# Performance work log

Hardware: AMD Instinct MI355X
Metric: run time of the kernel (lower is better)

## Reference

```python
import jax, jax.numpy as jnp
import numpy as np

NCHW = ('NCHW', 'OIHW', 'NCHW')


def _conv3x3_same(x, w, b):
    # ZeroPad2d(1) + 3x3 valid conv == 3x3 conv with padding 1
    y = jax.lax.conv_general_dilated(x, w, window_strides=(1, 1),
                                     padding=((1, 1), (1, 1)),
                                     dimension_numbers=NCHW)
    return y + b[None, :, None, None]


def _maxpool2(x):
    return jax.lax.reduce_window(x, -jnp.inf, jax.lax.max,
                                 (1, 1, 2, 2), (1, 1, 2, 2), 'VALID')


def setup_inputs() -> dict:
    key = jax.random.key(0)
    ks = jax.random.split(key, 12)
    B, T1, T2, R, D = 1, 512, 512, 9, 3840
    q = jax.random.normal(ks[0], (B, T1, R, D), jnp.float32)
    t = jax.random.normal(ks[1], (B, T2, R, D), jnp.float32)
    # ViSiL features are L2-normalized region descriptors -> sims in [-1,1]
    q = q / jnp.linalg.norm(q, axis=-1, keepdims=True)
    t = t / jnp.linalg.norm(t, axis=-1, keepdims=True)
    s = 0.05
    return {
        'query': q, 'target': t,
        'w1': jax.random.normal(ks[2], (32, 1, 3, 3), jnp.float32) * s,
        'b1': jax.random.normal(ks[3], (32,), jnp.float32) * s,
        'w2': jax.random.normal(ks[4], (64, 32, 3, 3), jnp.float32) * s,
        'b2': jax.random.normal(ks[5], (64,), jnp.float32) * s,
        'w3': jax.random.normal(ks[6], (128, 64, 3, 3), jnp.float32) * s,
        'b3': jax.random.normal(ks[7], (128,), jnp.float32) * s,
        'wf': jax.random.normal(ks[8], (1, 128, 1, 1), jnp.float32) * s,
        'bf': jax.random.normal(ks[9], (1,), jnp.float32) * s,
    }


def reference(query, target, w1, b1, w2, b2, w3, b3, wf, bf):
    # frame-to-frame: region-pair similarity [B,T1,O,P,T2]
    sim5 = jnp.einsum('biok,bjpk->biopj', query, target)
    # Chamfer (axes=[3,2]): max over target regions P, mean over query regions O
    f2f = jnp.mean(jnp.max(sim5, axis=3), axis=2)  # [B,T1,T2]
    # video comperator CNN
    x = f2f[:, None]                                 # [B,1,T1,T2]
    x = _maxpool2(jax.nn.relu(_conv3x3_same(x, w1, b1)))
    x = _maxpool2(jax.nn.relu(_conv3x3_same(x, w2, b2)))
    x = jax.nn.relu(_conv3x3_same(x, w3, b3))
    x = jax.lax.conv_general_dilated(x, wf, (1, 1), ((0, 0), (0, 0)),
                                     dimension_numbers=NCHW)
    x = x + bf[None, :, None, None]
    s = jnp.clip(x[:, 0], -1.0, 1.0)                 # Hardtanh, [B,H,W]
    # video-to-video Chamfer (axes=[2,1]): max over axis 2, mean over axis 1
    return jnp.mean(jnp.max(s, axis=2), axis=1)      # [B]
```

## Files before the change

### kernel.cpp

```cpp
#include <hip/hip_runtime.h>
#include <hip/hip_bf16.h>

typedef float f32x4 __attribute__((ext_vector_type(4)));
typedef int v8i __attribute__((ext_vector_type(8)));

#define AS3 __attribute__((address_space(3)))
#define AS1 __attribute__((address_space(1)))

__global__ __launch_bounds__(256) void cvt_fp8_kernel(const float* __restrict__ src,
                                                      unsigned int* __restrict__ dst,
                                                      int n16) {
  int idx = blockIdx.x * 256 + threadIdx.x;
  if (idx >= n16) return;
  const float4* s4 = (const float4*)src;
  uint4 o;
  unsigned int* op = (unsigned int*)&o;
#pragma unroll
  for (int i = 0; i < 4; ++i) {
    float4 v = s4[idx * 4 + i];
    int w = 0;
    w = __builtin_amdgcn_cvt_pk_fp8_f32(v.x * 16.f, v.y * 16.f, w, false);
    w = __builtin_amdgcn_cvt_pk_fp8_f32(v.z * 16.f, v.w * 16.f, w, true);
    op[i] = w;
  }
  ((uint4*)dst)[idx] = o;
}

__global__ __launch_bounds__(768) void gemm_cmax_kernel(const unsigned char* __restrict__ qf8,
                                                        const unsigned char* __restrict__ tf8,
                                                        float* __restrict__ cmax) {
  __shared__ __align__(16) char smem[147456];
  const int tid  = threadIdx.x;
  const int wv   = tid >> 6;
  const int lane = tid & 63;
  const int quad = lane >> 4;
  const int l16  = lane & 15;
  const int wrow = wv >> 1, wcol = wv & 1;
  const int bi = blockIdx.y, bj = blockIdx.x;

  f32x4 acc[3][9];
#pragma unroll
  for (int a = 0; a < 3; ++a)
#pragma unroll
    for (int b = 0; b < 9; ++b) acc[a][b] = (f32x4){0.f, 0.f, 0.f, 0.f};

  const unsigned char* gptr[6];
#pragma unroll
  for (int r = 0; r < 6; ++r) {
    int s   = r * 768 + wv * 64 + lane;
    int mat = (s >= 2304);
    int sm  = s - mat * 2304;
    int row = sm >> 3, pc = sm & 7;
    int gc  = pc ^ (row & 7);
    const unsigned char* base = mat ? (tf8 + (size_t)(bj * 288 + row) * 3840)
                                    : (qf8 + (size_t)(bi * 288 + row) * 3840);
    gptr[r] = base + gc * 16;
  }

  int buf = 0;
#pragma unroll
  for (int r = 0; r < 6; ++r)
    __builtin_amdgcn_global_load_lds((const AS1 void*)(gptr[r]),
                                     (AS3 void*)(smem + (r * 768 + wv * 64) * 16), 16, 0, 0);

  const int arow0 = wrow * 48 + l16;
  const int bcol0 = wcol * 144 + l16;

  for (int kt = 0; kt < 30; ++kt) {
    __syncthreads();
    if (kt < 29) {
      int nb = buf ^ 1;
#pragma unroll
      for (int r = 0; r < 6; ++r)
        __builtin_amdgcn_global_load_lds((const AS1 void*)(gptr[r] + (kt + 1) * 128),
                                         (AS3 void*)(smem + nb * 73728 + (r * 768 + wv * 64) * 16),
                                         16, 0, 0);
    }
    const char* A = smem + buf * 73728;
    const char* B = A + 36864;

    v8i av[3];
#pragma unroll
    for (int sr = 0; sr < 3; ++sr) {
      int row = arow0 + sr * 16;
      int sw  = row & 7;
      int p0  = (quad * 2) ^ sw, p1 = (quad * 2 + 1) ^ sw;
      int4 lo = *(const int4*)(A + row * 128 + p0 * 16);
      int4 hi = *(const int4*)(A + row * 128 + p1 * 16);
      v8i v;
      v[0] = lo.x; v[1] = lo.y; v[2] = lo.z; v[3] = lo.w;
      v[4] = hi.x; v[5] = hi.y; v[6] = hi.z; v[7] = hi.w;
      av[sr] = v;
    }
#pragma unroll
    for (int c = 0; c < 9; ++c) {
      int col = bcol0 + c * 16;
      int sw  = col & 7;
      int p0  = (quad * 2) ^ sw, p1 = (quad * 2 + 1) ^ sw;
      int4 lo = *(const int4*)(B + col * 128 + p0 * 16);
      int4 hi = *(const int4*)(B + col * 128 + p1 * 16);
      v8i bv;
      bv[0] = lo.x; bv[1] = lo.y; bv[2] = lo.z; bv[3] = lo.w;
      bv[4] = hi.x; bv[5] = hi.y; bv[6] = hi.z; bv[7] = hi.w;
      acc[0][c] = __builtin_amdgcn_mfma_scale_f32_16x16x128_f8f6f4(
          av[0], bv, acc[0][c], 0, 0, 0, 0x7f7f7f7f, 0, 0x7f7f7f7f);
      acc[1][c] = __builtin_amdgcn_mfma_scale_f32_16x16x128_f8f6f4(
          av[1], bv, acc[1][c], 0, 0, 0, 0x7f7f7f7f, 0, 0x7f7f7f7f);
      acc[2][c] = __builtin_amdgcn_mfma_scale_f32_16x16x128_f8f6f4(
          av[2], bv, acc[2][c], 0, 0, 0, 0x7f7f7f7f, 0, 0x7f7f7f7f);
    }
    buf ^= 1;
  }

  __syncthreads();
  float* scr = (float*)smem;
#pragma unroll
  for (int b = 0; b < 18; ++b) {
    const int bw = b / 3, bs = b - bw * 3;
    if (wrow == bw) {
#pragma unroll
      for (int c = 0; c < 9; ++c)
#pragma unroll
        for (int r = 0; r < 4; ++r)
          scr[(quad * 4 + r) * 288 + wcol * 144 + c * 16 + l16] = acc[bs][c][r] * (1.f / 256.f);
    }
    __syncthreads();
    if (tid < 512) {
      int row = tid >> 5, jg = tid & 31;
      const float* p = scr + row * 288 + jg * 9;
      float m = p[0];
#pragma unroll
      for (int k = 1; k < 9; ++k) m = fmaxf(m, p[k]);
      cmax[(size_t)(bi * 288 + b * 16 + row) * 512 + bj * 32 + jg] = m;
    }
    __syncthreads();
  }
}

__global__ __launch_bounds__(512) void mean9_kernel(const float* __restrict__ cmax,
                                                    float* __restrict__ f2f) {
  int i = blockIdx.x, j = threadIdx.x;
  float s = 0.f;
#pragma unroll
  for (int o = 0; o < 9; ++o) s += cmax[(size_t)(i * 9 + o) * 512 + j];
  f2f[i * 512 + j] = s * (1.f / 9.f);
}

__global__ __launch_bounds__(256) void conv1_kernel(const float* __restrict__ in,
                                                    const float* __restrict__ w1,
                                                    const float* __restrict__ b1,
                                                    float* __restrict__ out) {
  __shared__ float tile[34 * 36];
  __shared__ float wl[320];
  int t = blockIdx.x;
  int ty0 = (t >> 4) * 32, tx0 = (t & 15) * 32;
  int py = threadIdx.x >> 4, px = threadIdx.x & 15;

  for (int idx = threadIdx.x; idx < 320; idx += 256)
    wl[idx] = (idx < 288) ? w1[idx] : b1[idx - 288];
  for (int idx = threadIdx.x; idx < 34 * 34; idx += 256) {
    int r = idx / 34, c = idx % 34;
    int gy = ty0 + r - 1, gx = tx0 + c - 1;
    tile[r * 36 + c] = ((unsigned)gy < 512u && (unsigned)gx < 512u) ? in[gy * 512 + gx] : 0.f;
  }
  __syncthreads();

  float win[4][4];
#pragma unroll
  for (int r = 0; r < 4; ++r)
#pragma unroll
    for (int c = 0; c < 4; ++c)
      win[r][c] = tile[(2 * py + r) * 36 + 2 * px + c];

  int gy2 = (t >> 4) * 16 + py, gx2 = (t & 15) * 16 + px;
#pragma unroll 1
  for (int ch = 0; ch < 32; ++ch) {
    float w[9];
#pragma unroll
    for (int k = 0; k < 9; ++k) w[k] = wl[ch * 9 + k];
    float m = -INFINITY;
#pragma unroll
    for (int a = 0; a < 2; ++a)
#pragma unroll
      for (int b = 0; b < 2; ++b) {
        float s = 0.f;
#pragma unroll
        for (int ky = 0; ky < 3; ++ky)
#pragma unroll
          for (int kx = 0; kx < 3; ++kx) s += win[a + ky][b + kx] * w[ky * 3 + kx];
        m = fmaxf(m, s);
      }
    out[ch * 65536 + gy2 * 256 + gx2] = fmaxf(m + wl[288 + ch], 0.f);
  }
}

__global__ __launch_bounds__(256) void conv2_kernel(const float* __restrict__ in,
                                                    const float* __restrict__ w2,
                                                    const float* __restrict__ b2,
                                                    float* __restrict__ out) {
  __shared__ __align__(16) float wlds[32 * 4 * 12];
  __shared__ float tile[2][2][34 * 36];
  const int tid = threadIdx.x;
  int cog = blockIdx.x >> 6;
  int t   = blockIdx.x & 63;
  int ty0 = (t >> 3) * 32, tx0 = (t & 7) * 32;
  int py = tid >> 4, px = tid & 15;

  for (int idx = tid; idx < 1152; idx += 256) {
    int co = idx / 288, rem = idx % 288, ci = rem / 9, k = rem % 9;
    wlds[(ci * 4 + co) * 12 + k] = w2[((cog * 4 + co) * 32 + ci) * 9 + k];
  }
  for (int idx = tid; idx < 2312; idx += 256) {
    int pl = idx / 1156, rc = idx % 1156, r = rc / 34, c = rc % 34;
    int gy = ty0 + r - 1, gx = tx0 + c - 1;
    tile[0][pl][r * 36 + c] = ((unsigned)gy < 256u && (unsigned)gx < 256u)
                                  ? in[pl * 65536 + gy * 256 + gx] : 0.f;
  }
  __syncthreads();

  float acc[4][4];
#pragma unroll
  for (int p = 0; p < 4; ++p)
#pragma unroll
    for (int co = 0; co < 4; ++co) acc[p][co] = 0.f;

#pragma unroll 1
  for (int cb = 0; cb < 16; ++cb) {
    int buf = cb & 1;
    float pf[10];
    if (cb < 15) {
#pragma unroll
      for (int i = 0; i < 10; ++i) {
        int idx = tid + i * 256;
        float v = 0.f;
        if (idx < 2312) {
          int pl = idx / 1156, rc = idx % 1156, r = rc / 34, c = rc % 34;
          int gy = ty0 + r - 1, gx = tx0 + c - 1;
          if ((unsigned)gy < 256u && (unsigned)gx < 256u)
            v = in[((cb + 1) * 2 + pl) * 65536 + gy * 256 + gx];
        }
        pf[i] = v;
      }
    }
#pragma unroll
    for (int pl = 0; pl < 2; ++pl) {
      float win[4][4];
#pragma unroll
      for (int r = 0; r < 4; ++r) {
        float2 lo = *(const float2*)&tile[buf][pl][(2 * py + r) * 36 + 2 * px];
        float2 hi = *(const float2*)&tile[buf][pl][(2 * py + r) * 36 + 2 * px + 2];
        win[r][0] = lo.x; win[r][1] = lo.y; win[r][2] = hi.x; win[r][3] = hi.y;
      }
      int ci = cb * 2 + pl;
#pragma unroll
      for (int co = 0; co < 4; ++co) {
        const float* wp = &wlds[(ci * 4 + co) * 12];
        float4 w0 = *(const float4*)wp;
        float4 w1v = *(const float4*)(wp + 4);
        float w8 = wp[8];
        float w[9] = {w0.x, w0.y, w0.z, w0.w, w1v.x, w1v.y, w1v.z, w1v.w, w8};
#pragma unroll
        for (int a = 0; a < 2; ++a)
#pragma unroll
          for (int b = 0; b < 2; ++b) {
            float s = acc[a * 2 + b][co];
#pragma unroll
            for (int ky = 0; ky < 3; ++ky)
#pragma unroll
              for (int kx = 0; kx < 3; ++kx) s += win[a + ky][b + kx] * w[ky * 3 + kx];
            acc[a * 2 + b][co] = s;
          }
      }
    }
    if (cb < 15) {
#pragma unroll
      for (int i = 0; i < 10; ++i) {
        int idx = tid + i * 256;
        if (idx < 2312) {
          int pl = idx / 1156, rc = idx % 1156, r = rc / 34, c = rc % 34;
          tile[buf ^ 1][pl][r * 36 + c] = pf[i];
        }
      }
    }
    __syncthreads();
  }

  int gy2 = (t >> 3) * 16 + py, gx2 = (t & 7) * 16 + px;
#pragma unroll
  for (int co = 0; co < 4; ++co) {
    float m = fmaxf(fmaxf(acc[0][co], acc[1][co]), fmaxf(acc[2][co], acc[3][co]));
    out[(cog * 4 + co) * 16384 + gy2 * 128 + gx2] = fmaxf(m + b2[cog * 4 + co], 0.f);
  }
}

__global__ __launch_bounds__(256) void conv3_kernel(const float* __restrict__ in,
                                                    const float* __restrict__ w3,
                                                    const float* __restrict__ b3,
                                                    float* __restrict__ out) {
  __shared__ __align__(16) float wlds[64 * 4 * 12];
  __shared__ float tile[2][4][34 * 36];
  const int tid = threadIdx.x;
  int cog = blockIdx.x >> 4;
  int t   = blockIdx.x & 15;
  int ty0 = (t >> 2) * 32, tx0 = (t & 3) * 32;
  int py = tid >> 4, px = tid & 15;

  for (int idx = tid; idx < 2304; idx += 256) {
    int co = idx / 576, rem = idx % 576, ci = rem / 9, k = rem % 9;
    wlds[(ci * 4 + co) * 12 + k] = w3[((cog * 4 + co) * 64 + ci) * 9 + k];
  }
  for (int idx = tid; idx < 4624; idx += 256) {
    int pl = idx / 1156, rc = idx % 1156, r = rc / 34, c = rc % 34;
    int gy = ty0 + r - 1, gx = tx0 + c - 1;
    tile[0][pl][r * 36 + c] = ((unsigned)gy < 128u && (unsigned)gx < 128u)
                                  ? in[pl * 16384 + gy * 128 + gx] : 0.f;
  }
  __syncthreads();

  float acc[4][4];
#pragma unroll
  for (int p = 0; p < 4; ++p)
#pragma unroll
    for (int co = 0; co < 4; ++co) acc[p][co] = 0.f;

#pragma unroll 1
  for (int cb = 0; cb < 16; ++cb) {
    int buf = cb & 1;
    float pf[19];
    if (cb < 15) {
#pragma unroll
      for (int i = 0; i < 19; ++i) {
        int idx = tid + i * 256;
        float v = 0.f;
        if (idx < 4624) {
          int pl = idx / 1156, rc = idx % 1156, r = rc / 34, c = rc % 34;
          int gy = ty0 + r - 1, gx = tx0 + c - 1;
          if ((unsigned)gy < 128u && (unsigned)gx < 128u)
            v = in[((cb + 1) * 4 + pl) * 16384 + gy * 128 + gx];
        }
        pf[i] = v;
      }
    }
#pragma unroll
    for (int pl = 0; pl < 4; ++pl) {
      float win[4][4];
#pragma unroll
      for (int r = 0; r < 4; ++r) {
        float2 lo = *(const float2*)&tile[buf][pl][(2 * py + r) * 36 + 2 * px];
        float2 hi = *(const float2*)&tile[buf][pl][(2 * py + r) * 36 + 2 * px + 2];
        win[r][0] = lo.x; win[r][1] = lo.y; win[r][2] = hi.x; win[r][3] = hi.y;
      }
      int ci = cb * 4 + pl;
#pragma unroll
      for (int co = 0; co < 4; ++co) {
        const float* wp = &wlds[(ci * 4 + co) * 12];
        float4 w0 = *(const float4*)wp;
        float4 w1v = *(const float4*)(wp + 4);
        float w8 = wp[8];
        float w[9] = {w0.x, w0.y, w0.z, w0.w, w1v.x, w1v.y, w1v.z, w1v.w, w8};
#pragma unroll
        for (int a = 0; a < 2; ++a)
#pragma unroll
          for (int b = 0; b < 2; ++b) {
            float s = acc[a * 2 + b][co];
#pragma unroll
            for (int ky = 0; ky < 3; ++ky)
#pragma unroll
              for (int kx = 0; kx < 3; ++kx) s += win[a + ky][b + kx] * w[ky * 3 + kx];
            acc[a * 2 + b][co] = s;
          }
      }
    }
    if (cb < 15) {
#pragma unroll
      for (int i = 0; i < 19; ++i) {
        int idx = tid + i * 256;
        if (idx < 4624) {
          int pl = idx / 1156, rc = idx % 1156, r = rc / 34, c = rc % 34;
          tile[buf ^ 1][pl][r * 36 + c] = pf[i];
        }
      }
    }
    __syncthreads();
  }

#pragma unroll
  for (int co = 0; co < 4; ++co) {
    float bias = b3[cog * 4 + co];
    float* op = out + (cog * 4 + co) * 16384;
#pragma unroll
    for (int a = 0; a < 2; ++a)
#pragma unroll
      for (int b = 0; b < 2; ++b)
        op[(ty0 + 2 * py + a) * 128 + tx0 + 2 * px + b] = fmaxf(acc[a * 2 + b][co] + bias, 0.f);
  }
}

__global__ __launch_bounds__(512) void convf_kernel(const float* __restrict__ in,
                                                    const float* __restrict__ wf,
                                                    const float* __restrict__ bfp,
                                                    float* __restrict__ rowm) {
  __shared__ float part[512];
  int y = blockIdx.x, tid = threadIdx.x;
  int pt = tid >> 7, x = tid & 127;
  float acc = 0.f;
  const float* ip = in + y * 128 + x;
  for (int ci = pt * 32; ci < pt * 32 + 32; ++ci) acc += ip[ci * 16384] * wf[ci];
  part[tid] = acc;
  __syncthreads();
  if (tid < 128) {
    float s = part[tid] + part[tid + 128] + part[tid + 256] + part[tid + 384] + bfp[0];
    part[tid] = fminf(fmaxf(s, -1.f), 1.f);
  }
  __syncthreads();
  if (tid < 64) {
    float m = fmaxf(part[tid], part[tid + 64]);
    for (int off = 32; off; off >>= 1) m = fmaxf(m, __shfl_down(m, off, 64));
    if (tid == 0) rowm[y] = m;
  }
}

__global__ __launch_bounds__(128) void final_kernel(const float* __restrict__ rowm,
                                                    float* __restrict__ out) {
  int x = threadIdx.x;
  float v = rowm[x];
  for (int off = 32; off; off >>= 1) v += __shfl_down(v, off, 64);
  __shared__ float red[2];
  if ((x & 63) == 0) red[x >> 6] = v;
  __syncthreads();
  if (x == 0) out[0] = (red[0] + red[1]) * (1.f / 128.f);
}

extern "C" void kernel_launch(void* const* d_in, const int* in_sizes, int n_in,
                              void* d_out, int out_size, void* d_ws, size_t ws_size,
                              hipStream_t stream) {
  const float* q  = (const float*)d_in[0];
  const float* t  = (const float*)d_in[1];
  const float* w1 = (const float*)d_in[2];
  const float* b1 = (const float*)d_in[3];
  const float* w2 = (const float*)d_in[4];
  const float* b2 = (const float*)d_in[5];
  const float* w3 = (const float*)d_in[6];
  const float* b3 = (const float*)d_in[7];
  const float* wf = (const float*)d_in[8];
  const float* bf = (const float*)d_in[9];
  float* out = (float*)d_out;
  char* ws = (char*)d_ws;

  unsigned char* qf8 = (unsigned char*)(ws + 0);
  unsigned char* tf8 = (unsigned char*)(ws + 17694720);
  float* cmax = (float*)(ws + 35389440);
  float* f2f  = (float*)(ws + 44826624);
  float* x1   = (float*)(ws + 45875200);
  float* x2b  = (float*)(ws + 54263808);
  float* x3   = (float*)(ws + 58458112);
  float* rowm = (float*)(ws + 66846720);

  cvt_fp8_kernel<<<4320, 256, 0, stream>>>(q, (unsigned int*)qf8, 1105920);
  cvt_fp8_kernel<<<4320, 256, 0, stream>>>(t, (unsigned int*)tf8, 1105920);
  gemm_cmax_kernel<<<dim3(16, 16), 768, 0, stream>>>(qf8, tf8, cmax);
  mean9_kernel<<<512, 512, 0, stream>>>(cmax, f2f);
  conv1_kernel<<<256, 256, 0, stream>>>(f2f, w1, b1, x1);
  conv2_kernel<<<1024, 256, 0, stream>>>(x1, w2, b2, x2b);
  conv3_kernel<<<512, 256, 0, stream>>>(x2b, w3, b3, x3);
  convf_kernel<<<128, 512, 0, stream>>>(x3, wf, bf, rowm);
  final_kernel<<<1, 128, 0, stream>>>(rowm, out);
}
```

Before: 444.4 us.

## Merge fp8 conversions, remap GEMM block order, restripe conv2/conv3 with row-sliding windows

```diff
diff --git a/kernel.cpp b/kernel.cpp
--- a/kernel.cpp
+++ b/kernel.cpp
@@ -7,11 +7,16 @@
 #define AS3 __attribute__((address_space(3)))
 #define AS1 __attribute__((address_space(1)))
 
-__global__ __launch_bounds__(256) void cvt_fp8_kernel(const float* __restrict__ src,
-                                                      unsigned int* __restrict__ dst,
+__global__ __launch_bounds__(256) void cvt_fp8_kernel(const float* __restrict__ q,
+                                                      const float* __restrict__ t,
+                                                      unsigned int* __restrict__ qd,
+                                                      unsigned int* __restrict__ td,
                                                       int n16) {
   int idx = blockIdx.x * 256 + threadIdx.x;
-  if (idx >= n16) return;
+  const float* src;
+  unsigned int* dst;
+  if (idx < n16) { src = q; dst = qd; }
+  else           { idx -= n16; if (idx >= n16) return; src = t; dst = td; }
   const float4* s4 = (const float4*)src;
   uint4 o;
   unsigned int* op = (unsigned int*)&o;
@@ -36,7 +41,9 @@
   const int quad = lane >> 4;
   const int l16  = lane & 15;
   const int wrow = wv >> 1, wcol = wv & 1;
-  const int bi = blockIdx.y, bj = blockIdx.x;
+  const int x = blockIdx.x & 7, r = blockIdx.x >> 3;
+  const int bi = (x >> 1) * 4 + (r & 3);
+  const int bj = (x & 1) * 8 + (r >> 2);
 
   f32x4 acc[3][9];
 #pragma unroll
@@ -46,22 +53,22 @@
 
   const unsigned char* gptr[6];
 #pragma unroll
-  for (int r = 0; r < 6; ++r) {
-    int s   = r * 768 + wv * 64 + lane;
+  for (int i = 0; i < 6; ++i) {
+    int s   = i * 768 + wv * 64 + lane;
     int mat = (s >= 2304);
     int sm  = s - mat * 2304;
     int row = sm >> 3, pc = sm & 7;
     int gc  = pc ^ (row & 7);
     const unsigned char* base = mat ? (tf8 + (size_t)(bj * 288 + row) * 3840)
                                     : (qf8 + (size_t)(bi * 288 + row) * 3840);
-    gptr[r] = base + gc * 16;
+    gptr[i] = base + gc * 16;
   }
 
   int buf = 0;
 #pragma unroll
-  for (int r = 0; r < 6; ++r)
-    __builtin_amdgcn_global_load_lds((const AS1 void*)(gptr[r]),
-                                     (AS3 void*)(smem + (r * 768 + wv * 64) * 16), 16, 0, 0);
+  for (int i = 0; i < 6; ++i)
+    __builtin_amdgcn_global_load_lds((const AS1 void*)(gptr[i]),
+                                     (AS3 void*)(smem + (i * 768 + wv * 64) * 16), 16, 0, 0);
 
   const int arow0 = wrow * 48 + l16;
   const int bcol0 = wcol * 144 + l16;
@@ -71,9 +78,9 @@
     if (kt < 29) {
       int nb = buf ^ 1;
 #pragma unroll
-      for (int r = 0; r < 6; ++r)
-        __builtin_amdgcn_global_load_lds((const AS1 void*)(gptr[r] + (kt + 1) * 128),
-                                         (AS3 void*)(smem + nb * 73728 + (r * 768 + wv * 64) * 16),
+      for (int i = 0; i < 6; ++i)
+        __builtin_amdgcn_global_load_lds((const AS1 void*)(gptr[i] + (kt + 1) * 128),
+                                         (AS3 void*)(smem + nb * 73728 + (i * 768 + wv * 64) * 16),
                                          16, 0, 0);
     }
     const char* A = smem + buf * 73728;
@@ -121,8 +128,8 @@
 #pragma unroll
       for (int c = 0; c < 9; ++c)
 #pragma unroll
-        for (int r = 0; r < 4; ++r)
-          scr[(quad * 4 + r) * 288 + wcol * 144 + c * 16 + l16] = acc[bs][c][r] * (1.f / 256.f);
+        for (int rr = 0; rr < 4; ++rr)
+          scr[(quad * 4 + rr) * 288 + wcol * 144 + c * 16 + l16] = acc[bs][c][rr] * (1.f / 256.f);
     }
     __syncthreads();
     if (tid < 512) {
@@ -199,97 +206,107 @@
                                                     const float* __restrict__ b2,
                                                     float* __restrict__ out) {
   __shared__ __align__(16) float wlds[32 * 4 * 12];
-  __shared__ float tile[2][2][34 * 36];
+  __shared__ __align__(16) float tile[2 * 2 * 18 * 264];
   const int tid = threadIdx.x;
-  int cog = blockIdx.x >> 6;
-  int t   = blockIdx.x & 63;
-  int ty0 = (t >> 3) * 32, tx0 = (t & 7) * 32;
-  int py = tid >> 4, px = tid & 15;
+  const int stripe = blockIdx.x & 15, cog = blockIdx.x >> 4;
+  const int X = tid;
+  const int Y0 = stripe * 16;
 
   for (int idx = tid; idx < 1152; idx += 256) {
     int co = idx / 288, rem = idx % 288, ci = rem / 9, k = rem % 9;
     wlds[(ci * 4 + co) * 12 + k] = w2[((cog * 4 + co) * 32 + ci) * 9 + k];
   }
-  for (int idx = tid; idx < 2312; idx += 256) {
-    int pl = idx / 1156, rc = idx % 1156, r = rc / 34, c = rc % 34;
-    int gy = ty0 + r - 1, gx = tx0 + c - 1;
-    tile[0][pl][r * 36 + c] = ((unsigned)gy < 256u && (unsigned)gx < 256u)
-                                  ? in[pl * 65536 + gy * 256 + gx] : 0.f;
-  }
-  __syncthreads();
-
-  float acc[4][4];
-#pragma unroll
-  for (int p = 0; p < 4; ++p)
-#pragma unroll
-    for (int co = 0; co < 4; ++co) acc[p][co] = 0.f;
+  if (tid < 144) {
+    int bu = tid / 72, rem = tid % 72, pl = rem / 36, r2 = rem % 36;
+    int rr = r2 >> 1, side = r2 & 1;
+    tile[bu * 9504 + pl * 4752 + rr * 264 + (side ? 260 : 3)] = 0.f;
+  }
+  int gof[9], lof[9];
+#pragma unroll
+  for (int i = 0; i < 9; ++i) {
+    int idx = tid + i * 256;
+    int rw = idx >> 6, c4 = idx & 63;
+    int pl = (rw >= 18), rr = rw - pl * 18;
+    int gy = Y0 + rr - 1;
+    lof[i] = pl * 4752 + rr * 264 + 4 + c4 * 4;
+    gof[i] = ((unsigned)gy < 256u) ? (pl * 65536 + gy * 256 + c4 * 4) : -1;
+  }
+#pragma unroll
+  for (int i = 0; i < 9; ++i) {
+    float4 v = (gof[i] >= 0) ? *(const float4*)(in + gof[i]) : (float4){0, 0, 0, 0};
+    *(float4*)&tile[lof[i]] = v;
+  }
+  __syncthreads();
+
+  float acc[16][4];
+#pragma unroll
+  for (int y = 0; y < 16; ++y)
+#pragma unroll
+    for (int co = 0; co < 4; ++co) acc[y][co] = 0.f;
 
 #pragma unroll 1
   for (int cb = 0; cb < 16; ++cb) {
     int buf = cb & 1;
-    float pf[10];
+    float4 pf[9];
     if (cb < 15) {
 #pragma unroll
-      for (int i = 0; i < 10; ++i) {
-        int idx = tid + i * 256;
-        float v = 0.f;
-        if (idx < 2312) {
-          int pl = idx / 1156, rc = idx % 1156, r = rc / 34, c = rc % 34;
-          int gy = ty0 + r - 1, gx = tx0 + c - 1;
-          if ((unsigned)gy < 256u && (unsigned)gx < 256u)
-            v = in[((cb + 1) * 2 + pl) * 65536 + gy * 256 + gx];
-        }
-        pf[i] = v;
-      }
-    }
+      for (int i = 0; i < 9; ++i)
+        pf[i] = (gof[i] >= 0) ? *(const float4*)(in + gof[i] + (cb + 1) * 131072)
+                              : (float4){0, 0, 0, 0};
+    }
+    const float* tb = tile + buf * 9504;
 #pragma unroll
     for (int pl = 0; pl < 2; ++pl) {
-      float win[4][4];
-#pragma unroll
-      for (int r = 0; r < 4; ++r) {
-        float2 lo = *(const float2*)&tile[buf][pl][(2 * py + r) * 36 + 2 * px];
-        float2 hi = *(const float2*)&tile[buf][pl][(2 * py + r) * 36 + 2 * px + 2];
-        win[r][0] = lo.x; win[r][1] = lo.y; win[r][2] = hi.x; win[r][3] = hi.y;
-      }
+      const float* tp = tb + pl * 4752;
       int ci = cb * 2 + pl;
+      float w[4][9];
 #pragma unroll
       for (int co = 0; co < 4; ++co) {
         const float* wp = &wlds[(ci * 4 + co) * 12];
         float4 w0 = *(const float4*)wp;
-        float4 w1v = *(const float4*)(wp + 4);
-        float w8 = wp[8];
-        float w[9] = {w0.x, w0.y, w0.z, w0.w, w1v.x, w1v.y, w1v.z, w1v.w, w8};
-#pragma unroll
-        for (int a = 0; a < 2; ++a)
-#pragma unroll
-          for (int b = 0; b < 2; ++b) {
-            float s = acc[a * 2 + b][co];
-#pragma unroll
-            for (int ky = 0; ky < 3; ++ky)
-#pragma unroll
-              for (int kx = 0; kx < 3; ++kx) s += win[a + ky][b + kx] * w[ky * 3 + kx];
-            acc[a * 2 + b][co] = s;
-          }
+        float4 w1 = *(const float4*)(wp + 4);
+        w[co][0] = w0.x; w[co][1] = w0.y; w[co][2] = w0.z; w[co][3] = w0.w;
+        w[co][4] = w1.x; w[co][5] = w1.y; w[co][6] = w1.z; w[co][7] = w1.w;
+        w[co][8] = wp[8];
       }
+      float r0[3], r1[3], r2[3];
+      const float* p0 = tp + X + 3;
+      r0[0] = p0[0]; r0[1] = p0[1]; r0[2] = p0[2];
+      const float* p1 = tp + 264 + X + 3;
+      r1[0] = p1[0]; r1[1] = p1[1]; r1[2] = p1[2];
+#pragma unroll
+      for (int y = 0; y < 16; ++y) {
+        const float* p2 = tp + (y + 2) * 264 + X + 3;
+        r2[0] = p2[0]; r2[1] = p2[1]; r2[2] = p2[2];
+#pragma unroll
+        for (int co = 0; co < 4; ++co)
+          acc[y][co] += r0[0] * w[co][0] + r0[1] * w[co][1] + r0[2] * w[co][2]
+                      + r1[0] * w[co][3] + r1[1] * w[co][4] + r1[2] * w[co][5]
+                      + r2[0] * w[co][6] + r2[1] * w[co][7] + r2[2] * w[co][8];
+        r0[0] = r1[0]; r0[1] = r1[1]; r0[2] = r1[2];
+        r1[0] = r2[0]; r1[1] = r2[1]; r1[2] = r2[2];
+      }
     }
     if (cb < 15) {
 #pragma unroll
-      for (int i = 0; i < 10; ++i) {
-        int idx = tid + i * 256;
-        if (idx < 2312) {
-          int pl = idx / 1156, rc = idx % 1156, r = rc / 34, c = rc % 34;
-          tile[buf ^ 1][pl][r * 36 + c] = pf[i];
-        }
-      }
+      for (int i = 0; i < 9; ++i)
+        *(float4*)&tile[(buf ^ 1) * 9504 + lof[i]] = pf[i];
     }
     __syncthreads();
   }
 
-  int gy2 = (t >> 3) * 16 + py, gx2 = (t & 7) * 16 + px;
+  int x2 = X >> 1;
 #pragma unroll
   for (int co = 0; co < 4; ++co) {
-    float m = fmaxf(fmaxf(acc[0][co], acc[1][co]), fmaxf(acc[2][co], acc[3][co]));
-    out[(cog * 4 + co) * 16384 + gy2 * 128 + gx2] = fmaxf(m + b2[cog * 4 + co], 0.f);
+    float bias = b2[cog * 4 + co];
+#pragma unroll
+    for (int y2 = 0; y2 < 8; ++y2) {
+      float v = fmaxf(acc[2 * y2][co], acc[2 * y2 + 1][co]);
+      v = fmaxf(v + bias, 0.f);
+      float o = fmaxf(v, __shfl_xor(v, 1, 64));
+      if ((X & 1) == 0)
+        out[(cog * 4 + co) * 16384 + (stripe * 8 + y2) * 128 + x2] = o;
+    }
   }
 }
 
@@ -298,88 +315,94 @@
                                                     const float* __restrict__ b3,
                                                     float* __restrict__ out) {
   __shared__ __align__(16) float wlds[64 * 4 * 12];
-  __shared__ float tile[2][4][34 * 36];
+  __shared__ __align__(16) float tile[2 * 2 * 18 * 136];
   const int tid = threadIdx.x;
-  int cog = blockIdx.x >> 4;
-  int t   = blockIdx.x & 15;
-  int ty0 = (t >> 2) * 32, tx0 = (t & 3) * 32;
-  int py = tid >> 4, px = tid & 15;
+  const int stripe = blockIdx.x & 7, cog = blockIdx.x >> 3;
+  const int X = tid & 127, yh = tid >> 7;
+  const int Y0 = stripe * 16;
 
   for (int idx = tid; idx < 2304; idx += 256) {
     int co = idx / 576, rem = idx % 576, ci = rem / 9, k = rem % 9;
     wlds[(ci * 4 + co) * 12 + k] = w3[((cog * 4 + co) * 64 + ci) * 9 + k];
   }
-  for (int idx = tid; idx < 4624; idx += 256) {
-    int pl = idx / 1156, rc = idx % 1156, r = rc / 34, c = rc % 34;
-    int gy = ty0 + r - 1, gx = tx0 + c - 1;
-    tile[0][pl][r * 36 + c] = ((unsigned)gy < 128u && (unsigned)gx < 128u)
-                                  ? in[pl * 16384 + gy * 128 + gx] : 0.f;
-  }
-  __syncthreads();
-
-  float acc[4][4];
-#pragma unroll
-  for (int p = 0; p < 4; ++p)
-#pragma unroll
-    for (int co = 0; co < 4; ++co) acc[p][co] = 0.f;
+  if (tid < 144) {
+    int bu = tid / 72, rem = tid % 72, pl = rem / 36, r2 = rem % 36;
+    int rr = r2 >> 1, side = r2 & 1;
+    tile[bu * 4896 + pl * 2448 + rr * 136 + (side ? 132 : 3)] = 0.f;
+  }
+  int gof[5], lof[5];
+#pragma unroll
+  for (int i = 0; i < 5; ++i) {
+    int idx = tid + i * 256;
+    if (idx < 1152) {
+      int rw = idx >> 5, c4 = idx & 31;
+      int pl = (rw >= 18), rr = rw - pl * 18;
+      int gy = Y0 + rr - 1;
+      lof[i] = pl * 2448 + rr * 136 + 4 + c4 * 4;
+      gof[i] = ((unsigned)gy < 128u) ? (pl * 16384 + gy * 128 + c4 * 4) : -1;
+    } else { lof[i] = -1; gof[i] = -1; }
+  }
+#pragma unroll
+  for (int i = 0; i < 5; ++i)
+    if (lof[i] >= 0) {
+      float4 v = (gof[i] >= 0) ? *(const float4*)(in + gof[i]) : (float4){0, 0, 0, 0};
+      *(float4*)&tile[lof[i]] = v;
+    }
+  __syncthreads();
+
+  float acc[8][4];
+#pragma unroll
+  for (int y = 0; y < 8; ++y)
+#pragma unroll
+    for (int co = 0; co < 4; ++co) acc[y][co] = 0.f;
 
 #pragma unroll 1
-  for (int cb = 0; cb < 16; ++cb) {
+  for (int cb = 0; cb < 32; ++cb) {
     int buf = cb & 1;
-    float pf[19];
-    if (cb < 15) {
-#pragma unroll
-      for (int i = 0; i < 19; ++i) {
-        int idx = tid + i * 256;
-        float v = 0.f;
-        if (idx < 4624) {
-          int pl = idx / 1156, rc = idx % 1156, r = rc / 34, c = rc % 34;
-          int gy = ty0 + r - 1, gx = tx0 + c - 1;
-          if ((unsigned)gy < 128u && (unsigned)gx < 128u)
-            v = in[((cb + 1) * 4 + pl) * 16384 + gy * 128 + gx];
-        }
-        pf[i] = v;
-      }
-    }
-#pragma unroll
-    for (int pl = 0; pl < 4; ++pl) {
-      float win[4][4];
-#pragma unroll
-      for (int r = 0; r < 4; ++r) {
-        float2 lo = *(const float2*)&tile[buf][pl][(2 * py + r) * 36 + 2 * px];
-        float2 hi = *(const float2*)&tile[buf][pl][(2 * py + r) * 36 + 2 * px + 2];
-        win[r][0] = lo.x; win[r][1] = lo.y; win[r][2] = hi.x; win[r][3] = hi.y;
-      }
-      int ci = cb * 4 + pl;
+    float4 pf[5];
+    if (cb < 31) {
+#pragma unroll
+      for (int i = 0; i < 5; ++i)
+        pf[i] = (gof[i] >= 0) ? *(const float4*)(in + gof[i] + (cb + 1) * 32768)
+                              : (float4){0, 0, 0, 0};
+    }
+    const float* tb = tile + buf * 4896;
+#pragma unroll
+    for (int pl = 0; pl < 2; ++pl) {
+      const float* tp = tb + pl * 2448;
+      int ci = cb * 2 + pl;
+      float w[4][9];
 #pragma unroll
       for (int co = 0; co < 4; ++co) {
         const float* wp = &wlds[(ci * 4 + co) * 12];
         float4 w0 = *(const float4*)wp;
-        float4 w1v = *(const float4*)(wp + 4);
-        float w8 = wp[8];
-        float w[9] = {w0.x, w0.y, w0.z, w0.w, w1v.x, w1v.y, w1v.z, w1v.w, w8};
-#pragma unroll
-        for (int a = 0; a < 2; ++a)
-#pragma unroll
-          for (int b = 0; b < 2; ++b) {
-            float s = acc[a * 2 + b][co];
-#pragma unroll
-            for (int ky = 0; ky < 3; ++ky)
-#pragma unroll
-              for (int kx = 0; kx < 3; ++kx) s += win[a + ky][b + kx] * w[ky * 3 + kx];
-            acc[a * 2 + b][co] = s;
-          }
+        float4 w1 = *(const float4*)(wp + 4);
+        w[co][0] = w0.x; w[co][1] = w0.y; w[co][2] = w0.z; w[co][3] = w0.w;
+        w[co][4] = w1.x; w[co][5] = w1.y; w[co][6] = w1.z; w[co][7] = w1.w;
+        w[co][8] = wp[8];
       }
-    }
-    if (cb < 15) {
-#pragma unroll
-      for (int i = 0; i < 19; ++i) {
-        int idx = tid + i * 256;
-        if (idx < 4624) {
-          int pl = idx / 1156, rc = idx % 1156, r = rc / 34, c = rc % 34;
-          tile[buf ^ 1][pl][r * 36 + c] = pf[i];
-        }
+      float r0[3], r1[3], r2[3];
+      const float* p0 = tp + (yh * 8) * 136 + X + 3;
+      r0[0] = p0[0]; r0[1] = p0[1]; r0[2] = p0[2];
+      const float* p1 = tp + (yh * 8 + 1) * 136 + X + 3;
+      r1[0] = p1[0]; r1[1] = p1[1]; r1[2] = p1[2];
+#pragma unroll
+      for (int y = 0; y < 8; ++y) {
+        const float* p2 = tp + (yh * 8 + y + 2) * 136 + X + 3;
+        r2[0] = p2[0]; r2[1] = p2[1]; r2[2] = p2[2];
+#pragma unroll
+        for (int co = 0; co < 4; ++co)
+          acc[y][co] += r0[0] * w[co][0] + r0[1] * w[co][1] + r0[2] * w[co][2]
+                      + r1[0] * w[co][3] + r1[1] * w[co][4] + r1[2] * w[co][5]
+                      + r2[0] * w[co][6] + r2[1] * w[co][7] + r2[2] * w[co][8];
+        r0[0] = r1[0]; r0[1] = r1[1]; r0[2] = r1[2];
+        r1[0] = r2[0]; r1[1] = r2[1]; r1[2] = r2[2];
       }
+    }
+    if (cb < 31) {
+#pragma unroll
+      for (int i = 0; i < 5; ++i)
+        if (lof[i] >= 0) *(float4*)&tile[(buf ^ 1) * 4896 + lof[i]] = pf[i];
     }
     __syncthreads();
   }
@@ -387,12 +410,10 @@
 #pragma unroll
   for (int co = 0; co < 4; ++co) {
     float bias = b3[cog * 4 + co];
-    float* op = out + (cog * 4 + co) * 16384;
-#pragma unroll
-    for (int a = 0; a < 2; ++a)
-#pragma unroll
-      for (int b = 0; b < 2; ++b)
-        op[(ty0 + 2 * py + a) * 128 + tx0 + 2 * px + b] = fmaxf(acc[a * 2 + b][co] + bias, 0.f);
+    float* op = out + (cog * 4 + co) * 16384 + (Y0 + yh * 8) * 128 + X;
+#pragma unroll
+    for (int y = 0; y < 8; ++y)
+      op[y * 128] = fmaxf(acc[y][co] + bias, 0.f);
   }
 }
 
@@ -456,13 +477,12 @@
   float* x3   = (float*)(ws + 58458112);
   float* rowm = (float*)(ws + 66846720);
 
-  cvt_fp8_kernel<<<4320, 256, 0, stream>>>(q, (unsigned int*)qf8, 1105920);
-  cvt_fp8_kernel<<<4320, 256, 0, stream>>>(t, (unsigned int*)tf8, 1105920);
-  gemm_cmax_kernel<<<dim3(16, 16), 768, 0, stream>>>(qf8, tf8, cmax);
+  cvt_fp8_kernel<<<8640, 256, 0, stream>>>(q, t, (unsigned int*)qf8, (unsigned int*)tf8, 1105920);
+  gemm_cmax_kernel<<<256, 768, 0, stream>>>(qf8, tf8, cmax);
   mean9_kernel<<<512, 512, 0, stream>>>(cmax, f2f);
   conv1_kernel<<<256, 256, 0, stream>>>(f2f, w1, b1, x1);
-  conv2_kernel<<<1024, 256, 0, stream>>>(x1, w2, b2, x2b);
-  conv3_kernel<<<512, 256, 0, stream>>>(x2b, w3, b3, x3);
+  conv2_kernel<<<256, 256, 0, stream>>>(x1, w2, b2, x2b);
+  conv3_kernel<<<256, 256, 0, stream>>>(x2b, w3, b3, x3);
   convf_kernel<<<128, 512, 0, stream>>>(x3, wf, bf, rowm);
   final_kernel<<<1, 128, 0, stream>>>(rowm, out);
 }
```

Result: faster. 406.8 us (-8.5%).
